# Optimization experiments

Measured on AMD Instinct MI355X. Metric: run time of the kernel, lower is better.

## Reference

```python
import jax, jax.numpy as jnp
import numpy as np
import math

CHANNEL = 512
NUM_HEAD = 8
HEAD_DIM = 64


def setup_inputs() -> dict:
    key = jax.random.key(0)
    ks = jax.random.split(key, 9)
    d = NUM_HEAD * HEAD_DIM  # 512
    s = 1.0 / math.sqrt(CHANNEL)
    return {
        "x": jax.random.normal(ks[0], (8, CHANNEL, 32, 32), dtype=jnp.float32),
        "wq": jax.random.normal(ks[1], (CHANNEL, d), dtype=jnp.float32) * s,
        "bq": jnp.zeros((d,), dtype=jnp.float32),
        "wk": jax.random.normal(ks[2], (CHANNEL, d), dtype=jnp.float32) * s,
        "bk": jnp.zeros((d,), dtype=jnp.float32),
        "wv": jax.random.normal(ks[3], (CHANNEL, d), dtype=jnp.float32) * s,
        "bv": jnp.zeros((d,), dtype=jnp.float32),
        "wo": jax.random.normal(ks[4], (d, CHANNEL), dtype=jnp.float32) * s,
        "bo": jnp.zeros((CHANNEL,), dtype=jnp.float32),
    }


def reference(x, wq, bq, wk, bk, wv, bv, wo, bo):
    B, C, H, W = x.shape
    S = H * W
    # [B, C, H, W] -> [B, S, C]
    xr = x.transpose(0, 2, 3, 1).reshape(B, S, C)
    q = (xr @ wq + bq).reshape(B, S, NUM_HEAD, HEAD_DIM)
    k = (xr @ wk + bk).reshape(B, S, NUM_HEAD, HEAD_DIM)
    v = (xr @ wv + bv).reshape(B, S, NUM_HEAD, HEAD_DIM)
    # NOTE: original scales by 1/sqrt(channel), not 1/sqrt(head_dim)
    energy = jnp.einsum('bqhd,bkhd->bhqk', q, k) / math.sqrt(C)
    attn = jax.nn.softmax(energy, axis=-1)
    out = jnp.einsum('bhqk,bkhd->bqhd', attn, v).reshape(B, S, NUM_HEAD * HEAD_DIM)
    out = out @ wo + bo  # [B, S, C]
    out = out.transpose(0, 2, 1).reshape(B, C, H, W)
    return x + out
```

## Files before the change

### kernel.cpp

```cpp
#include <hip/hip_runtime.h>
#include <hip/hip_bf16.h>

typedef __bf16 bf16_t;
typedef __attribute__((ext_vector_type(8))) __bf16 bf16x8;
typedef __attribute__((ext_vector_type(4))) __bf16 bf16x4;
typedef __attribute__((ext_vector_type(4))) float f32x4;

#define AS1 __attribute__((address_space(1)))
#define AS3 __attribute__((address_space(3)))

__device__ __forceinline__ void gload_lds16(const void* g, void* l) {
  __builtin_amdgcn_global_load_lds((const AS1 void*)g, (AS3 void*)l, 16, 0, 0);
}

__global__ void __launch_bounds__(256) prep_kernel(
    const float* __restrict__ x, const float* __restrict__ w0,
    const float* __restrict__ w1, const float* __restrict__ w2,
    const float* __restrict__ w3, bf16_t* __restrict__ xr, bf16_t* __restrict__ t0,
    bf16_t* __restrict__ t1, bf16_t* __restrict__ t2, bf16_t* __restrict__ t3) {
  __shared__ float tile[32][33];
  const int tx = threadIdx.x, ty = threadIdx.y;
  int t = blockIdx.x;
  const float* src;
  bf16_t* dst;
  int ld_src, ld_dst, r0, c0;
  if (t < 1024) {
    int z = t >> 8, rem = t & 255;
    src = (z == 0) ? w0 : (z == 1) ? w1 : (z == 2) ? w2 : w3;
    dst = (z == 0) ? t0 : (z == 1) ? t1 : (z == 2) ? t2 : t3;
    ld_src = 512; ld_dst = 512;
    r0 = (rem & 15) * 32; c0 = (rem >> 4) * 32;
  } else {
    t -= 1024;
    int b = t >> 9, rem = t & 511;
    src = x + (size_t)b * 512 * 1024;
    dst = xr + (size_t)b * 1024 * 512;
    ld_src = 1024; ld_dst = 512;
    r0 = (rem & 15) * 32; c0 = (rem >> 4) * 32;
  }
#pragma unroll
  for (int i = 0; i < 32; i += 8)
    tile[ty + i][tx] = src[(r0 + ty + i) * ld_src + c0 + tx];
  __syncthreads();
#pragma unroll
  for (int i = 0; i < 32; i += 8)
    dst[(c0 + ty + i) * ld_dst + r0 + tx] = (bf16_t)tile[tx][ty + i];
}

__device__ __forceinline__ void gemm_nt_128x128_p4(const bf16_t* __restrict__ Abase,
                                                   const bf16_t* __restrict__ Bbase,
                                                   bf16_t (*As)[128 * 32],
                                                   bf16_t (*Bs)[128 * 32],
                                                   f32x4 acc[4][4]) {
  const int tid = threadIdx.x;
  const int lane = tid & 63;
  const int wid = tid >> 6;
  const int wr = wid >> 1, wc = wid & 1;
  const int lrow = lane & 15;
  const int kgrp = lane >> 4;
  const int r0 = tid >> 2;
  const int cb = (tid & 3) * 16;

#pragma unroll
  for (int p = 0; p < 2; ++p) {
    const int kt = p * 32;
#pragma unroll
    for (int j = 0; j < 2; ++j) {
      int row = j * 64 + r0;
      gload_lds16((const char*)(Abase + row * 512 + kt) + cb, (char*)As[p] + row * 64 + cb);
    }
#pragma unroll
    for (int j = 0; j < 2; ++j) {
      int row = j * 64 + r0;
      gload_lds16((const char*)(Bbase + row * 512 + kt) + cb, (char*)Bs[p] + row * 64 + cb);
    }
  }

  for (int t = 0; t < 16; ++t) {
    const int cur = t & 3;
    if (t < 14) {
      const int nxt = (t + 2) & 3;
      const int kt = (t + 2) * 32;
#pragma unroll
      for (int j = 0; j < 2; ++j) {
        int row = j * 64 + r0;
        gload_lds16((const char*)(Abase + row * 512 + kt) + cb,
                    (char*)As[nxt] + row * 64 + cb);
      }
#pragma unroll
      for (int j = 0; j < 2; ++j) {
        int row = j * 64 + r0;
        gload_lds16((const char*)(Bbase + row * 512 + kt) + cb,
                    (char*)Bs[nxt] + row * 64 + cb);
      }
      asm volatile("s_waitcnt vmcnt(8)" ::: "memory");
    } else if (t == 14) {
      asm volatile("s_waitcnt vmcnt(4)" ::: "memory");
    } else {
      asm volatile("s_waitcnt vmcnt(0)" ::: "memory");
    }
    __builtin_amdgcn_sched_barrier(0);
    __builtin_amdgcn_s_barrier();

    bf16x8 a[4], b[4];
#pragma unroll
    for (int mf = 0; mf < 4; ++mf)
      a[mf] = *(const bf16x8*)(As[cur] + (wr * 64 + mf * 16 + lrow) * 32 + kgrp * 8);
#pragma unroll
    for (int nf = 0; nf < 4; ++nf)
      b[nf] = *(const bf16x8*)(Bs[cur] + (wc * 64 + nf * 16 + lrow) * 32 + kgrp * 8);
    __builtin_amdgcn_s_setprio(1);
#pragma unroll
    for (int mf = 0; mf < 4; ++mf)
#pragma unroll
      for (int nf = 0; nf < 4; ++nf)
        acc[mf][nf] = __builtin_amdgcn_mfma_f32_16x16x32_bf16(a[mf], b[nf], acc[mf][nf], 0, 0, 0);
    __builtin_amdgcn_s_setprio(0);
  }
}

__global__ void __launch_bounds__(256, 2) gemm_qkv_kernel(
    const bf16_t* __restrict__ xr, const bf16_t* __restrict__ wqT,
    const bf16_t* __restrict__ wkT, const bf16_t* __restrict__ wvT,
    const float* __restrict__ bq, const float* __restrict__ bk,
    const float* __restrict__ bv, bf16_t* __restrict__ qo, bf16_t* __restrict__ ko,
    bf16_t* __restrict__ vto) {
  __shared__ bf16_t As[4][128 * 32];
  __shared__ bf16_t Bs[4][128 * 32];
  const int bn = blockIdx.x, bm = blockIdx.y, z = blockIdx.z;
  const bf16_t* wT = (z == 0) ? wqT : (z == 1) ? wkT : wvT;
  const float* bias = (z == 0) ? bq : (z == 1) ? bk : bv;
  f32x4 acc[4][4] = {};
  gemm_nt_128x128_p4(xr + bm * 128 * 512, wT + bn * 128 * 512, As, Bs, acc);
  const int lane = threadIdx.x & 63, wid = threadIdx.x >> 6;
  const int lrow = lane & 15, kgrp = lane >> 4;
  const int wr = wid >> 1, wc = wid & 1;
  const int row0 = bm * 128 + wr * 64;
  const int col0 = bn * 128 + wc * 64;
  const float qscale = 0.044194173824159216f * 1.4426950408889634f;
  if (z == 2) {
#pragma unroll
    for (int mf = 0; mf < 4; ++mf)
#pragma unroll
      for (int nf = 0; nf < 4; ++nf) {
        int n = col0 + nf * 16 + lrow;
        int h = n >> 6, d = n & 63;
        float bb = bias[n];
        int m0 = row0 + mf * 16 + kgrp * 4;
        int b = m0 >> 10, s = m0 & 1023;
        bf16x4 pk;
#pragma unroll
        for (int r = 0; r < 4; ++r) pk[r] = (bf16_t)(acc[mf][nf][r] + bb);
        *(bf16x4*)(vto + (((size_t)(b * 8 + h) * 64 + d) * 1024 + s)) = pk;
      }
  } else {
    bf16_t* out = (z == 0) ? qo : ko;
    const float sc = (z == 0) ? qscale : 1.0f;
#pragma unroll
    for (int mf = 0; mf < 4; ++mf)
#pragma unroll
      for (int nf = 0; nf < 4; ++nf) {
        int n = col0 + nf * 16 + lrow;
        int h = n >> 6, d = n & 63;
        float bb = bias[n];
#pragma unroll
        for (int r = 0; r < 4; ++r) {
          int m = row0 + mf * 16 + kgrp * 4 + r;
          int b = m >> 10, s = m & 1023;
          out[((b * 8 + h) * 1024 + s) * 64 + d] = (bf16_t)((acc[mf][nf][r] + bb) * sc);
        }
      }
  }
}

__global__ void __launch_bounds__(256, 2) attn_kernel(const bf16_t* __restrict__ q,
                                                      const bf16_t* __restrict__ k,
                                                      const bf16_t* __restrict__ vt,
                                                      bf16_t* __restrict__ attn_out) {
  __shared__ char Ks[4][8192];
  __shared__ char Vs[4][8192];
  __shared__ char Ps[4][4096];
  const int tid = threadIdx.x;
  const int lane = tid & 63, wid = tid >> 6;
  const int lrow = lane & 15, kgrp = lane >> 4;
  const int bh = blockIdx.x, qb = blockIdx.y;
  const int b = bh >> 3, h = bh & 7;

  const char* khb = (const char*)(k + (size_t)bh * 1024 * 64);
  const char* vthb = (const char*)(vt + (size_t)bh * 64 * 1024);
  const bf16_t* qh = q + (size_t)bh * 1024 * 64;

  const int qbase = qb * 128 + wid * 32;
  bf16x8 qa[2][2];
#pragma unroll
  for (int qf = 0; qf < 2; ++qf) {
    int qrow = qbase + qf * 16 + lrow;
    qa[qf][0] = *(const bf16x8*)(qh + qrow * 64 + kgrp * 8);
    qa[qf][1] = *(const bf16x8*)(qh + qrow * 64 + 32 + kgrp * 8);
  }

  char* Pw = Ps[wid];
  const int srow = tid >> 3;
  const int sc2 = tid & 7;

  float l_part[2] = {0.f, 0.f};
  f32x4 o[2][4] = {};

#pragma unroll
  for (int p = 0; p < 2; ++p) {
    const char* kg = khb + p * (64 * 128);
    const char* vg = vthb + p * 128;
#pragma unroll
    for (int j = 0; j < 2; ++j) {
      int row = j * 32 + srow;
      gload_lds16(kg + row * 128 + ((sc2 ^ (row & 7)) * 16), Ks[p] + j * 4096 + tid * 16);
    }
#pragma unroll
    for (int j = 0; j < 2; ++j) {
      int row = j * 32 + srow;
      gload_lds16(vg + row * 2048 + ((sc2 ^ (row & 7)) * 16), Vs[p] + j * 4096 + tid * 16);
    }
  }

  for (int t = 0; t < 16; ++t) {
    const int cur = t & 3;
    if (t < 14) {
      const int nxt = (t + 2) & 3;
      const char* kg = khb + (t + 2) * (64 * 128);
      const char* vg = vthb + (t + 2) * 128;
#pragma unroll
      for (int j = 0; j < 2; ++j) {
        int row = j * 32 + srow;
        gload_lds16(kg + row * 128 + ((sc2 ^ (row & 7)) * 16),
                    Ks[nxt] + j * 4096 + tid * 16);
      }
#pragma unroll
      for (int j = 0; j < 2; ++j) {
        int row = j * 32 + srow;
        gload_lds16(vg + row * 2048 + ((sc2 ^ (row & 7)) * 16),
                    Vs[nxt] + j * 4096 + tid * 16);
      }
      asm volatile("s_waitcnt vmcnt(8)" ::: "memory");
    } else if (t == 14) {
      asm volatile("s_waitcnt vmcnt(4)" ::: "memory");
    } else {
      asm volatile("s_waitcnt vmcnt(0)" ::: "memory");
    }
    __builtin_amdgcn_sched_barrier(0);
    __builtin_amdgcn_s_barrier();

    const char* Kc = Ks[cur];
    const char* Vc = Vs[cur];

    f32x4 sa[2][4] = {};
    __builtin_amdgcn_s_setprio(1);
#pragma unroll
    for (int c = 0; c < 4; ++c) {
      int krow = c * 16 + lrow;
      bf16x8 k0 = *(const bf16x8*)(Kc + krow * 128 + ((kgrp ^ (krow & 7)) * 16));
      bf16x8 k1 = *(const bf16x8*)(Kc + krow * 128 + (((4 + kgrp) ^ (krow & 7)) * 16));
#pragma unroll
      for (int qf = 0; qf < 2; ++qf) {
        sa[qf][c] = __builtin_amdgcn_mfma_f32_16x16x32_bf16(k0, qa[qf][0], sa[qf][c], 0, 0, 0);
        sa[qf][c] = __builtin_amdgcn_mfma_f32_16x16x32_bf16(k1, qa[qf][1], sa[qf][c], 0, 0, 0);
      }
    }
    __builtin_amdgcn_s_setprio(0);

#pragma unroll
    for (int qf = 0; qf < 2; ++qf) {
      int prow = qf * 16 + lrow;
      float rs = 0.f;
#pragma unroll
      for (int c = 0; c < 4; ++c) {
        bf16x4 pk;
#pragma unroll
        for (int r = 0; r < 4; ++r) {
          float p = exp2f(sa[qf][c][r]);
          rs += p;
          pk[r] = (bf16_t)p;
        }
        int chunk = (c * 2 + (kgrp >> 1)) ^ (prow & 7);
        *(bf16x4*)(Pw + prow * 128 + chunk * 16 + (kgrp & 1) * 8) = pk;
      }
      l_part[qf] += rs;
    }

    __builtin_amdgcn_s_setprio(1);
#pragma unroll
    for (int kk = 0; kk < 2; ++kk) {
      bf16x8 pa[2];
#pragma unroll
      for (int qf = 0; qf < 2; ++qf) {
        int prow = qf * 16 + lrow;
        int pchunk = (kk * 4 + kgrp) ^ (prow & 7);
        pa[qf] = *(const bf16x8*)(Pw + prow * 128 + pchunk * 16);
      }
#pragma unroll
      for (int nfo = 0; nfo < 4; ++nfo) {
        int vrow = nfo * 16 + lrow;
        int vchunk = (kk * 4 + kgrp) ^ (vrow & 7);
        bf16x8 vb = *(const bf16x8*)(Vc + vrow * 128 + vchunk * 16);
#pragma unroll
        for (int qf = 0; qf < 2; ++qf)
          o[qf][nfo] = __builtin_amdgcn_mfma_f32_16x16x32_bf16(pa[qf], vb, o[qf][nfo], 0, 0, 0);
      }
    }
    __builtin_amdgcn_s_setprio(0);
  }

#pragma unroll
  for (int qf = 0; qf < 2; ++qf) {
    l_part[qf] += __shfl_xor(l_part[qf], 16, 64);
    l_part[qf] += __shfl_xor(l_part[qf], 32, 64);
  }
#pragma unroll
  for (int qf = 0; qf < 2; ++qf)
#pragma unroll
    for (int r = 0; r < 4; ++r) {
      float inv = 1.0f / __shfl(l_part[qf], kgrp * 4 + r, 64);
      int s = qbase + qf * 16 + kgrp * 4 + r;
#pragma unroll
      for (int nfo = 0; nfo < 4; ++nfo) {
        int d = nfo * 16 + lrow;
        attn_out[((b * 1024 + s) * 8 + h) * 64 + d] = (bf16_t)(o[qf][nfo][r] * inv);
      }
    }
}

__global__ void __launch_bounds__(256, 2) gemm_out_kernel(const bf16_t* __restrict__ woT,
                                                          const bf16_t* __restrict__ attn,
                                                          const float* __restrict__ x,
                                                          const float* __restrict__ bo,
                                                          float* __restrict__ out) {
  __shared__ bf16_t As[4][128 * 32];
  __shared__ bf16_t Bs[4][128 * 32];
  const int bn = blockIdx.x, bm = blockIdx.y;
  f32x4 acc[4][4] = {};
  gemm_nt_128x128_p4(woT + bm * 128 * 512, attn + bn * 128 * 512, As, Bs, acc);
  const int lane = threadIdx.x & 63, wid = threadIdx.x >> 6;
  const int wr = wid >> 1, wc = wid & 1;
  const int c0 = bm * 128 + wr * 64;
  const int s0g = bn * 128 + wc * 64;
#pragma unroll
  for (int mf = 0; mf < 4; ++mf)
#pragma unroll
    for (int r = 0; r < 4; ++r) {
      int c = c0 + mf * 16 + (lane >> 4) * 4 + r;
      float bias = bo[c];
#pragma unroll
      for (int nf = 0; nf < 4; ++nf) {
        int n = s0g + nf * 16 + (lane & 15);
        int b = n >> 10, s = n & 1023;
        int idx = (b * 512 + c) * 1024 + s;
        out[idx] = x[idx] + acc[mf][nf][r] + bias;
      }
    }
}

extern "C" void kernel_launch(void* const* d_in, const int* in_sizes, int n_in,
                              void* d_out, int out_size, void* d_ws, size_t ws_size,
                              hipStream_t stream) {
  const float* x  = (const float*)d_in[0];
  const float* wq = (const float*)d_in[1];
  const float* bq = (const float*)d_in[2];
  const float* wk = (const float*)d_in[3];
  const float* bk = (const float*)d_in[4];
  const float* wv = (const float*)d_in[5];
  const float* bv = (const float*)d_in[6];
  const float* wo = (const float*)d_in[7];
  const float* bo = (const float*)d_in[8];
  float* out = (float*)d_out;

  char* ws = (char*)d_ws;
  const size_t SZ_XR = (size_t)8192 * 512 * 2;
  const size_t SZ_W  = (size_t)512 * 512 * 2;
  const size_t SZ_T  = (size_t)8 * 8 * 1024 * 64 * 2;
  bf16_t* xr   = (bf16_t*)(ws);
  bf16_t* wqT  = (bf16_t*)(ws + SZ_XR);
  bf16_t* wkT  = (bf16_t*)(ws + SZ_XR + SZ_W);
  bf16_t* wvT  = (bf16_t*)(ws + SZ_XR + 2 * SZ_W);
  bf16_t* woT  = (bf16_t*)(ws + SZ_XR + 3 * SZ_W);
  bf16_t* qd   = (bf16_t*)(ws + SZ_XR + 4 * SZ_W);
  bf16_t* kd   = (bf16_t*)(ws + SZ_XR + 4 * SZ_W + SZ_T);
  bf16_t* vtd  = (bf16_t*)(ws + SZ_XR + 4 * SZ_W + 2 * SZ_T);
  bf16_t* attn = (bf16_t*)(ws);

  prep_kernel<<<dim3(5120), dim3(32, 8), 0, stream>>>(x, wq, wk, wv, wo, xr, wqT, wkT,
                                                      wvT, woT);
  gemm_qkv_kernel<<<dim3(4, 64, 3), 256, 0, stream>>>(xr, wqT, wkT, wvT, bq, bk, bv,
                                                      qd, kd, vtd);
  attn_kernel<<<dim3(64, 8), 256, 0, stream>>>(qd, kd, vtd, attn);
  gemm_out_kernel<<<dim3(64, 4), 256, 0, stream>>>(woT, attn, x, bo, out);
}
```

Before: 85.43 us.

## Widen QKV GEMM tile to 128x256 with 3-stage pipeline over concatenated weights

The QKV projection now treats the three transposed weight matrices as one contiguous 1536-row matrix and computes 128x256 output tiles, which halves how often the A tile is reloaded per output column. The grid becomes 6x64 blocks and the LDS pipeline drops from 4 stages to 3 to fit the larger B tile. Each thread now holds twice as many accumulators, which raises register pressure and may lower occupancy. It relies on wqT/wkT/wvT being adjacent in the workspace, which the existing layout provides.

```diff
diff --git a/kernel.cpp b/kernel.cpp
--- a/kernel.cpp
+++ b/kernel.cpp
@@ -119,33 +119,108 @@
   }
 }
 
+__device__ __forceinline__ void gemm_nt_128x256_p3(const bf16_t* __restrict__ Abase,
+                                                   const bf16_t* __restrict__ Bbase,
+                                                   bf16_t (*As)[128 * 32],
+                                                   bf16_t (*Bs)[256 * 32],
+                                                   f32x4 acc[4][8]) {
+  const int tid = threadIdx.x;
+  const int lane = tid & 63;
+  const int wid = tid >> 6;
+  const int wr = wid >> 1, wc = wid & 1;
+  const int lrow = lane & 15;
+  const int kgrp = lane >> 4;
+  const int r0 = tid >> 2;
+  const int cb = (tid & 3) * 16;
+
+#pragma unroll
+  for (int p = 0; p < 2; ++p) {
+    const int kt = p * 32;
+#pragma unroll
+    for (int j = 0; j < 2; ++j) {
+      int row = j * 64 + r0;
+      gload_lds16((const char*)(Abase + row * 512 + kt) + cb, (char*)As[p] + row * 64 + cb);
+    }
+#pragma unroll
+    for (int j = 0; j < 4; ++j) {
+      int row = j * 64 + r0;
+      gload_lds16((const char*)(Bbase + row * 512 + kt) + cb, (char*)Bs[p] + row * 64 + cb);
+    }
+  }
+  asm volatile("s_waitcnt vmcnt(6)" ::: "memory");
+  __builtin_amdgcn_sched_barrier(0);
+
+  int cur = 0, nxt = 2;
+  for (int t = 0; t < 16; ++t) {
+    __builtin_amdgcn_s_barrier();
+    __builtin_amdgcn_sched_barrier(0);
+    if (t < 14) {
+      const int kt = (t + 2) * 32;
+#pragma unroll
+      for (int j = 0; j < 2; ++j) {
+        int row = j * 64 + r0;
+        gload_lds16((const char*)(Abase + row * 512 + kt) + cb,
+                    (char*)As[nxt] + row * 64 + cb);
+      }
+#pragma unroll
+      for (int j = 0; j < 4; ++j) {
+        int row = j * 64 + r0;
+        gload_lds16((const char*)(Bbase + row * 512 + kt) + cb,
+                    (char*)Bs[nxt] + row * 64 + cb);
+      }
+    }
+
+    bf16x8 a[4], b[8];
+#pragma unroll
+    for (int mf = 0; mf < 4; ++mf)
+      a[mf] = *(const bf16x8*)(As[cur] + (wr * 64 + mf * 16 + lrow) * 32 + kgrp * 8);
+#pragma unroll
+    for (int nf = 0; nf < 8; ++nf)
+      b[nf] = *(const bf16x8*)(Bs[cur] + (wc * 128 + nf * 16 + lrow) * 32 + kgrp * 8);
+    __builtin_amdgcn_s_setprio(1);
+#pragma unroll
+    for (int mf = 0; mf < 4; ++mf)
+#pragma unroll
+      for (int nf = 0; nf < 8; ++nf)
+        acc[mf][nf] = __builtin_amdgcn_mfma_f32_16x16x32_bf16(a[mf], b[nf], acc[mf][nf], 0, 0, 0);
+    __builtin_amdgcn_s_setprio(0);
+    if (t < 14) {
+      asm volatile("s_waitcnt vmcnt(6)" ::: "memory");
+    } else {
+      asm volatile("s_waitcnt vmcnt(0)" ::: "memory");
+    }
+    __builtin_amdgcn_sched_barrier(0);
+    cur = (cur == 2) ? 0 : cur + 1;
+    nxt = (nxt == 2) ? 0 : nxt + 1;
+  }
+}
+
 __global__ void __launch_bounds__(256, 2) gemm_qkv_kernel(
-    const bf16_t* __restrict__ xr, const bf16_t* __restrict__ wqT,
-    const bf16_t* __restrict__ wkT, const bf16_t* __restrict__ wvT,
+    const bf16_t* __restrict__ xr, const bf16_t* __restrict__ wT ,
     const float* __restrict__ bq, const float* __restrict__ bk,
     const float* __restrict__ bv, bf16_t* __restrict__ qo, bf16_t* __restrict__ ko,
     bf16_t* __restrict__ vto) {
-  __shared__ bf16_t As[4][128 * 32];
-  __shared__ bf16_t Bs[4][128 * 32];
-  const int bn = blockIdx.x, bm = blockIdx.y, z = blockIdx.z;
-  const bf16_t* wT = (z == 0) ? wqT : (z == 1) ? wkT : wvT;
+  __shared__ bf16_t As[3][128 * 32];
+  __shared__ bf16_t Bs[3][256 * 32];
+  const int bn = blockIdx.x, bm = blockIdx.y;
+  const int z = bn >> 1;
   const float* bias = (z == 0) ? bq : (z == 1) ? bk : bv;
-  f32x4 acc[4][4] = {};
-  gemm_nt_128x128_p4(xr + bm * 128 * 512, wT + bn * 128 * 512, As, Bs, acc);
+  f32x4 acc[4][8] = {};
+  gemm_nt_128x256_p3(xr + bm * 128 * 512, wT + (size_t)bn * 256 * 512, As, Bs, acc);
   const int lane = threadIdx.x & 63, wid = threadIdx.x >> 6;
   const int lrow = lane & 15, kgrp = lane >> 4;
   const int wr = wid >> 1, wc = wid & 1;
   const int row0 = bm * 128 + wr * 64;
-  const int col0 = bn * 128 + wc * 64;
+  const int col0 = bn * 256 + wc * 128;
   const float qscale = 0.044194173824159216f * 1.4426950408889634f;
   if (z == 2) {
 #pragma unroll
     for (int mf = 0; mf < 4; ++mf)
 #pragma unroll
-      for (int nf = 0; nf < 4; ++nf) {
-        int n = col0 + nf * 16 + lrow;
-        int h = n >> 6, d = n & 63;
-        float bb = bias[n];
+      for (int nf = 0; nf < 8; ++nf) {
+        int nl = (col0 + nf * 16 + lrow) & 511;
+        int h = nl >> 6, d = nl & 63;
+        float bb = bias[nl];
         int m0 = row0 + mf * 16 + kgrp * 4;
         int b = m0 >> 10, s = m0 & 1023;
         bf16x4 pk;
@@ -159,10 +234,10 @@
 #pragma unroll
     for (int mf = 0; mf < 4; ++mf)
 #pragma unroll
-      for (int nf = 0; nf < 4; ++nf) {
-        int n = col0 + nf * 16 + lrow;
-        int h = n >> 6, d = n & 63;
-        float bb = bias[n];
+      for (int nf = 0; nf < 8; ++nf) {
+        int nl = (col0 + nf * 16 + lrow) & 511;
+        int h = nl >> 6, d = nl & 63;
+        float bb = bias[nl];
 #pragma unroll
         for (int r = 0; r < 4; ++r) {
           int m = row0 + mf * 16 + kgrp * 4 + r;
@@ -388,8 +463,7 @@
 
   prep_kernel<<<dim3(5120), dim3(32, 8), 0, stream>>>(x, wq, wk, wv, wo, xr, wqT, wkT,
                                                       wvT, woT);
-  gemm_qkv_kernel<<<dim3(4, 64, 3), 256, 0, stream>>>(xr, wqT, wkT, wvT, bq, bk, bv,
-                                                      qd, kd, vtd);
+  gemm_qkv_kernel<<<dim3(6, 64), 256, 0, stream>>>(xr, wqT, bq, bk, bv, qd, kd, vtd);
   attn_kernel<<<dim3(64, 8), 256, 0, stream>>>(qd, kd, vtd, attn);
   gemm_out_kernel<<<dim3(64, 4), 256, 0, stream>>>(woT, attn, x, bo, out);
 }
```

After: 85.26 us. Within noise of the previous version (-0.2%).
